# Kernel optimization log

Hardware: AMD Instinct MI355X
Metric: run time of the kernel (lower is better)

## Reference

```python
import jax, jax.numpy as jnp
import numpy as np
from jax import lax

H = 512   # hidden_size
O = 256   # output_size
B = 64    # batch
S = 1024  # encoder sequence length
T = 256   # decoder timesteps


def setup_inputs() -> dict:
    key = jax.random.key(0)
    ks = jax.random.split(key, 10)
    bound = 1.0 / np.sqrt(H)  # PyTorch LSTM/Linear init scale
    return {
        "encoder_outputs": jax.random.normal(ks[0], (B, S, H), jnp.float32),
        "hidden": jax.random.normal(ks[1], (1, B, H), jnp.float32),
        "cell": jax.random.normal(ks[2], (1, B, H), jnp.float32),
        "target": jax.random.normal(ks[3], (B, T, O), jnp.float32),
        # LSTM params (gate order i, f, g, o as in PyTorch)
        "W_ih": jax.random.uniform(ks[4], (4 * H, H + O), jnp.float32, -bound, bound),
        "W_hh": jax.random.uniform(ks[5], (4 * H, H), jnp.float32, -bound, bound),
        "b_ih": jax.random.uniform(ks[6], (4 * H,), jnp.float32, -bound, bound),
        "b_hh": jax.random.uniform(ks[7], (4 * H,), jnp.float32, -bound, bound),
        # FC params
        "W_fc": jax.random.uniform(ks[8], (O, H), jnp.float32, -bound, bound),
        "b_fc": jax.random.uniform(ks[9], (O,), jnp.float32, -bound, bound),
    }


def reference(encoder_outputs, hidden, cell, target, W_ih, W_hh, b_ih, b_hh, W_fc, b_fc):
    h0 = hidden[0]  # [B, H]
    c0 = cell[0]    # [B, H]

    def step(carry, x_t):
        h, c = carry
        # Attention: dot-product scores over encoder positions
        scores = jnp.einsum("bsh,bh->bs", encoder_outputs, h)      # [B, S]
        attn = jax.nn.softmax(scores, axis=1)
        context = jnp.einsum("bs,bsh->bh", attn, encoder_outputs)  # [B, H]
        x = jnp.concatenate([context, x_t], axis=-1)               # [B, H+O]
        # Single-step LSTM cell (PyTorch gate order i, f, g, o)
        gates = x @ W_ih.T + b_ih + h @ W_hh.T + b_hh              # [B, 4H]
        i_g, f_g, g_g, o_g = jnp.split(gates, 4, axis=-1)
        i_g = jax.nn.sigmoid(i_g)
        f_g = jax.nn.sigmoid(f_g)
        g_g = jnp.tanh(g_g)
        o_g = jax.nn.sigmoid(o_g)
        c_new = f_g * c + i_g * g_g
        h_new = o_g * jnp.tanh(c_new)
        out = h_new @ W_fc.T + b_fc                                # [B, O]
        return (h_new, c_new), out

    _, outs = lax.scan(step, (h0, c0), jnp.swapaxes(target, 0, 1))  # outs: [T, B, O]
    return jnp.swapaxes(outs, 0, 1)  # [B, T, O]
```

## Files before the change

kernel.cpp:

```cpp
#include <hip/hip_runtime.h>

#define HH 512
#define OO 256
#define BB 64
#define SS 1024
#define TT 256
#define KK 1280

typedef __attribute__((ext_vector_type(8))) short bh8;
typedef __attribute__((ext_vector_type(8))) _Float16 hf8;
typedef __attribute__((ext_vector_type(2))) _Float16 h2;
typedef __attribute__((ext_vector_type(4))) float fx4;
typedef unsigned short ushort_t;

__device__ __forceinline__ ushort_t f2bf(float x) {
    union { float f; unsigned int u; } v; v.f = x;
    unsigned int r = v.u + 0x7fffu + ((v.u >> 16) & 1u);
    return (ushort_t)(r >> 16);
}
__device__ __forceinline__ float bf2f(ushort_t s) {
    union { unsigned int u; float f; } z; z.u = ((unsigned int)s) << 16; return z.f;
}

__global__ void prep_weights(const float* __restrict__ W_ih,
                             const float* __restrict__ W_hh,
                             ushort_t* __restrict__ wfH,
                             ushort_t* __restrict__ wfL) {
    int g = blockIdx.x * 256 + threadIdx.x;
    if (g >= 64 * 40 * 2 * 64) return;
    int lane = g & 63;
    int nt = (g >> 6) & 1;
    int kk = (g >> 7) % 40;
    int ht = (g >> 7) / 40;
    int c = nt * 16 + (lane & 15);
    int gate = c >> 3, rr = c & 7;
    int j = gate * 512 + ht * 8 + rr;
    int kbase = kk * 32 + (lane >> 4) * 8;
    ushort_t* dh = wfH + (size_t)g * 8;
    ushort_t* dl = wfL + (size_t)g * 8;
#pragma unroll
    for (int r = 0; r < 8; ++r) {
        int k = kbase + r;
        float v = (k < 768) ? W_ih[(size_t)j * 768 + k]
                            : W_hh[(size_t)j * 512 + (k - 768)];
        ushort_t hi = f2bf(v);
        dh[r] = hi;
        dl[r] = f2bf(v - bf2f(hi));
    }
}

__global__ void prep_misc(const float* __restrict__ hidden,
                          const float* __restrict__ cell,
                          const float* __restrict__ W_fc,
                          float* __restrict__ h, float* __restrict__ c,
                          _Float16* __restrict__ wfc16) {
    const int total = 32768 + 32768 + 131072;
    for (int i = blockIdx.x * 256 + threadIdx.x; i < total; i += gridDim.x * 256) {
        if (i < 32768)       h[i] = hidden[i];
        else if (i < 65536)  c[i - 32768] = cell[i - 32768];
        else                 wfc16[i - 65536] = (_Float16)W_fc[i - 65536];
    }
}

__global__ void prep_ench(const float* __restrict__ enc,
                          _Float16* __restrict__ ench) {
    const size_t i = ((size_t)blockIdx.x * 256 + threadIdx.x) * 8;
    const float4 a = *(const float4*)(enc + i);
    const float4 b = *(const float4*)(enc + i + 4);
    hf8 o;
    o[0] = (_Float16)a.x; o[1] = (_Float16)a.y;
    o[2] = (_Float16)a.z; o[3] = (_Float16)a.w;
    o[4] = (_Float16)b.x; o[5] = (_Float16)b.y;
    o[6] = (_Float16)b.z; o[7] = (_Float16)b.w;
    *(hf8*)(ench + i) = o;
}

__device__ __forceinline__ void fc_unit(int v, int tprev,
                                        const float* __restrict__ h,
                                        const _Float16* __restrict__ wfc16,
                                        const float* __restrict__ b_fc,
                                        float* __restrict__ out,
                                        float (*shacc)[64]) {
    const int tid = threadIdx.x;
    const int b = v >> 2, oq = v & 3;
    const int ol = tid & 63, kq = tid >> 6;
    const int o = oq * 64 + ol;
    float acc = 0.f;
    const float* hp = h + b * HH + kq * 128;
    const _Float16* wp = wfc16 + (size_t)o * HH + kq * 128;
#pragma unroll 8
    for (int k2 = 0; k2 < 128; ++k2) acc += hp[k2] * (float)wp[k2];
    shacc[kq][ol] = acc;
    __syncthreads();
    if (tid < 64) {
        float vv = shacc[0][tid] + shacc[1][tid]
                 + shacc[2][tid] + shacc[3][tid] + b_fc[oq * 64 + tid];
        out[((size_t)b * TT + tprev) * OO + oq * 64 + tid] = vv;
    }
}

__global__ void __launch_bounds__(256)
step_attnp(int t, const _Float16* __restrict__ ench,
           const float* __restrict__ h,
           float* __restrict__ pm, float* __restrict__ pl,
           _Float16* __restrict__ pctx,
           const _Float16* __restrict__ wfc16, const float* __restrict__ b_fc,
           float* __restrict__ out) {
    const int tid = threadIdx.x;
    const int lane = tid & 63;
    const int w = tid >> 6;

    __shared__ union {
        struct { float m[4]; float l[4]; float ctx[4][512]; } a;
        struct { float acc[4][64]; } o;
    } sh;

    const int u = blockIdx.x;
    if (u < 1024) {
        const int b = u >> 4, ch = u & 15;
        float m = -3.0e38f, l = 0.f;
        const float* hb = h + b * HH + lane * 8;
        h2 hp[4];
#pragma unroll
        for (int i = 0; i < 4; ++i)
            hp[i] = (h2){(_Float16)hb[2 * i], (_Float16)hb[2 * i + 1]};
        float cx[8];
#pragma unroll
        for (int j = 0; j < 8; ++j) cx[j] = 0.f;
        const _Float16* er =
            ench + ((size_t)(b * SS + ch * 64 + w * 16)) * HH + lane * 8;
        for (int g4 = 0; g4 < 4; ++g4) {
            const hf8 v0 = *(const hf8*)er;
            const hf8 v1 = *(const hf8*)(er + HH);
            const hf8 v2 = *(const hf8*)(er + 2 * HH);
            const hf8 v3 = *(const hf8*)(er + 3 * HH);
            const h2* q0 = (const h2*)&v0;
            const h2* q1 = (const h2*)&v1;
            const h2* q2 = (const h2*)&v2;
            const h2* q3 = (const h2*)&v3;
            float d0 = 0.f, d1 = 0.f, d2 = 0.f, d3 = 0.f;
#pragma unroll
            for (int i = 0; i < 4; ++i) {
                d0 = __builtin_amdgcn_fdot2(q0[i], hp[i], d0, false);
                d1 = __builtin_amdgcn_fdot2(q1[i], hp[i], d1, false);
                d2 = __builtin_amdgcn_fdot2(q2[i], hp[i], d2, false);
                d3 = __builtin_amdgcn_fdot2(q3[i], hp[i], d3, false);
            }
#pragma unroll
            for (int off = 32; off; off >>= 1) {
                d0 += __shfl_xor(d0, off);
                d1 += __shfl_xor(d1, off);
                d2 += __shfl_xor(d2, off);
                d3 += __shfl_xor(d3, off);
            }
            const float mx = fmaxf(fmaxf(d0, d1), fmaxf(d2, d3));
            if (mx > m) {
                const float fs = __expf(m - mx);
                l *= fs;
#pragma unroll
                for (int j = 0; j < 8; ++j) cx[j] *= fs;
                m = mx;
            }
            const float p0 = __expf(d0 - m);
            const float p1 = __expf(d1 - m);
            const float p2 = __expf(d2 - m);
            const float p3 = __expf(d3 - m);
            l += (p0 + p1) + (p2 + p3);
            const h2 pk01 = (h2){(_Float16)p0, (_Float16)p1};
            const h2 pk23 = (h2){(_Float16)p2, (_Float16)p3};
#pragma unroll
            for (int j = 0; j < 8; ++j) {
                cx[j] = __builtin_amdgcn_fdot2((h2){v0[j], v1[j]}, pk01, cx[j], false);
                cx[j] = __builtin_amdgcn_fdot2((h2){v2[j], v3[j]}, pk23, cx[j], false);
            }
            er += 4 * HH;
        }
        if (lane == 0) { sh.a.m[w] = m; sh.a.l[w] = l; }
        *(float4*)&sh.a.ctx[w][lane * 8]     = make_float4(cx[0], cx[1], cx[2], cx[3]);
        *(float4*)&sh.a.ctx[w][lane * 8 + 4] = make_float4(cx[4], cx[5], cx[6], cx[7]);
        __syncthreads();
        float M = fmaxf(fmaxf(sh.a.m[0], sh.a.m[1]), fmaxf(sh.a.m[2], sh.a.m[3]));
        float wg[4]; float ls = 0.f;
#pragma unroll
        for (int q = 0; q < 4; ++q) { wg[q] = __expf(sh.a.m[q] - M); ls += wg[q] * sh.a.l[q]; }
        const int hh = tid * 2;
        float v0 = wg[0] * sh.a.ctx[0][hh] + wg[1] * sh.a.ctx[1][hh]
                 + wg[2] * sh.a.ctx[2][hh] + wg[3] * sh.a.ctx[3][hh];
        float v1 = wg[0] * sh.a.ctx[0][hh + 1] + wg[1] * sh.a.ctx[1][hh + 1]
                 + wg[2] * sh.a.ctx[2][hh + 1] + wg[3] * sh.a.ctx[3][hh + 1];
        _Float16* pc = pctx + ((size_t)(b * 16 + ch)) * HH;
        pc[hh]     = (_Float16)v0;
        pc[hh + 1] = (_Float16)v1;
        if (tid == 0) { pm[b * 16 + ch] = M; pl[b * 16 + ch] = ls; }
    } else if (t > 0) {
        fc_unit(u - 1024, t - 1, h, wfc16, b_fc, out, sh.o.acc);
    }
}

__global__ void __launch_bounds__(256)
step_combine(int t, const float* __restrict__ target, const float* __restrict__ h,
             const float* __restrict__ pm, const float* __restrict__ pl,
             const _Float16* __restrict__ pctx,
             ushort_t* __restrict__ xbh, ushort_t* __restrict__ xbl) {
    const int tid = threadIdx.x;
    const int b = blockIdx.x >> 1, hf = blockIdx.x & 1;
    float Mb = -3.0e38f;
#pragma unroll
    for (int q2 = 0; q2 < 16; ++q2) Mb = fmaxf(Mb, pm[b * 16 + q2]);
    float wq[16]; float lsb = 0.f;
#pragma unroll
    for (int q2 = 0; q2 < 16; ++q2) {
        wq[q2] = __expf(pm[b * 16 + q2] - Mb);
        lsb += wq[q2] * pl[b * 16 + q2];
    }
    const float inv = 1.0f / lsb;
    const int col = hf * 256 + tid;
    float s = 0.f;
#pragma unroll
    for (int q2 = 0; q2 < 16; ++q2)
        s += wq[q2] * (float)pctx[((size_t)(b * 16 + q2)) * HH + col];
    s *= inv;
    const ushort_t a0 = f2bf(s);
    xbh[b * KK + col] = a0;
    xbl[b * KK + col] = f2bf(s - bf2f(a0));
    if (hf == 0) {
        const float tv = target[((size_t)b * TT + t) * OO + tid];
        const ushort_t t0 = f2bf(tv);
        xbh[b * KK + 512 + tid] = t0;
        xbl[b * KK + 512 + tid] = f2bf(tv - bf2f(t0));
    } else {
        const int h2i = tid * 2;
        const float hv0 = h[b * HH + h2i], hv1 = h[b * HH + h2i + 1];
        const ushort_t g0 = f2bf(hv0), g1 = f2bf(hv1);
        xbh[b * KK + 768 + h2i]     = g0;
        xbl[b * KK + 768 + h2i]     = f2bf(hv0 - bf2f(g0));
        xbh[b * KK + 768 + h2i + 1] = g1;
        xbl[b * KK + 768 + h2i + 1] = f2bf(hv1 - bf2f(g1));
    }
}

__global__ void __launch_bounds__(256)
step_gates(const ushort_t* __restrict__ xbh,
           const ushort_t* __restrict__ xbl,
           const ushort_t* __restrict__ wfH,
           const ushort_t* __restrict__ wfL,
           const float* __restrict__ b_ih, const float* __restrict__ b_hh,
           float* __restrict__ h, float* __restrict__ c) {
    const int tid = threadIdx.x;
    const int lane = tid & 63;
    const int w = tid >> 6;
    __shared__ float g[32][32];

    const int bh = blockIdx.x >> 6;
    const int ht = blockIdx.x & 63;
    const int nt = w >> 1;
    fx4 a0 = {0, 0, 0, 0};
    const int bro = bh * 32 + 16 * (w & 1) + (lane & 15);
    const int kg = lane >> 4;
    const size_t wbase = (size_t)ht * 40 * 2 * 512;
    for (int kk = 0; kk < 40; ++kk) {
        const size_t aoff = (size_t)bro * KK + kk * 32 + kg * 8;
        bh8 avh = *(const bh8*)(xbh + aoff);
        bh8 avl = *(const bh8*)(xbl + aoff);
        bh8 bhv = *(const bh8*)(wfH + wbase + (kk * 2 + nt) * 512 + lane * 8);
        bh8 blv = *(const bh8*)(wfL + wbase + (kk * 2 + nt) * 512 + lane * 8);
        a0 = __builtin_amdgcn_mfma_f32_16x16x32_bf16(avh, bhv, a0, 0, 0, 0);
        a0 = __builtin_amdgcn_mfma_f32_16x16x32_bf16(avl, bhv, a0, 0, 0, 0);
        a0 = __builtin_amdgcn_mfma_f32_16x16x32_bf16(avh, blv, a0, 0, 0, 0);
    }
    const int crow = (lane >> 4) * 4;
#pragma unroll
    for (int r = 0; r < 4; ++r)
        g[16 * (w & 1) + crow + r][nt * 16 + (lane & 15)] = a0[r];
    __syncthreads();
    {
        const int lb = tid >> 3, r = tid & 7;
        const int b = bh * 32 + lb;
        const int hidx = ht * 8 + r;
        float gi = g[lb][r]      + b_ih[hidx]        + b_hh[hidx];
        float gf = g[lb][8 + r]  + b_ih[512 + hidx]  + b_hh[512 + hidx];
        float gg = g[lb][16 + r] + b_ih[1024 + hidx] + b_hh[1024 + hidx];
        float go = g[lb][24 + r] + b_ih[1536 + hidx] + b_hh[1536 + hidx];
        float ig = 1.f / (1.f + __expf(-gi));
        float fg = 1.f / (1.f + __expf(-gf));
        float g2 = tanhf(gg);
        float og = 1.f / (1.f + __expf(-go));
        float cn = fg * c[b * HH + hidx] + ig * g2;
        float hn = og * tanhf(cn);
        c[b * HH + hidx] = cn;
        h[b * HH + hidx] = hn;
    }
}

__global__ void __launch_bounds__(256)
fc_final(const float* __restrict__ h, const _Float16* __restrict__ wfc16,
         const float* __restrict__ b_fc, float* __restrict__ out) {
    __shared__ float acc[4][64];
    fc_unit(blockIdx.x, TT - 1, h, wfc16, b_fc, out, acc);
}

extern "C" void kernel_launch(void* const* d_in, const int* in_sizes, int n_in,
                              void* d_out, int out_size, void* d_ws, size_t ws_size,
                              hipStream_t stream) {
    const float* enc    = (const float*)d_in[0];
    const float* hidden = (const float*)d_in[1];
    const float* cellp  = (const float*)d_in[2];
    const float* target = (const float*)d_in[3];
    const float* W_ih   = (const float*)d_in[4];
    const float* W_hh   = (const float*)d_in[5];
    const float* b_ih   = (const float*)d_in[6];
    const float* b_hh   = (const float*)d_in[7];
    const float* W_fc   = (const float*)d_in[8];
    const float* b_fc   = (const float*)d_in[9];
    float* out = (float*)d_out;

    char* base = (char*)d_ws;
    float* h            = (float*)(base + 0);
    float* c            = (float*)(base + 131072);
    ushort_t* wfH       = (ushort_t*)(base + 262144);
    ushort_t* wfL       = (ushort_t*)(base + 5505024);
    ushort_t* xbh       = (ushort_t*)(base + 10747904);
    ushort_t* xbl       = (ushort_t*)(base + 10911744);
    float* pm           = (float*)(base + 11075584);
    float* pl           = (float*)(base + 11079680);
    _Float16* wfc16     = (_Float16*)(base + 11083776);
    _Float16* pctx      = (_Float16*)(base + 11345920);
    _Float16* ench      = (_Float16*)(base + 12394496);

    prep_weights<<<dim3(1280), dim3(256), 0, stream>>>(W_ih, W_hh, wfH, wfL);
    prep_misc<<<dim3(768), dim3(256), 0, stream>>>(hidden, cellp, W_fc, h, c, wfc16);
    prep_ench<<<dim3(16384), dim3(256), 0, stream>>>(enc, ench);

    for (int t = 0; t < TT; ++t) {
        step_attnp<<<dim3(1280), dim3(256), 0, stream>>>(
            t, ench, h, pm, pl, pctx, wfc16, b_fc, out);
        step_combine<<<dim3(128), dim3(256), 0, stream>>>(
            t, target, h, pm, pl, pctx, xbh, xbl);
        step_gates<<<dim3(128), dim3(256), 0, stream>>>(
            xbh, xbl, wfH, wfL, b_ih, b_hh, h, c);
    }
    fc_final<<<dim3(256), dim3(256), 0, stream>>>(h, wfc16, b_fc, out);
}
```

Baseline: 8.680 ms.

## Fuse attention-context combine into gate GEMM and precompute target/hidden gate partials

Removes the per-step combine kernel. The target and previous-h contributions to the gates are now computed as extra blocks inside the attention launch, using the split-bf16 MFMA path, and written to a partial-gates buffer. The gate kernel applies the softmax rescaling to each of the 16 partial contexts and multiplies them by a new fp16 copy of the context half of W_ih, accumulating onto those partials. This cuts one launch per timestep and the round trip through the x staging buffers, at the cost of repeating the context MFMA work 16 times, lower context-path precision (single fp16 instead of hi/lo bf16), and a leftover redundant prep_weights call with unused pointer variables.

```diff
diff --git a/kernel.cpp b/kernel.cpp
--- a/kernel.cpp
+++ b/kernel.cpp
@@ -47,6 +47,24 @@
         dh[r] = hi;
         dl[r] = f2bf(v - bf2f(hi));
     }
+}
+
+__global__ void prep_wc16(const float* __restrict__ W_ih,
+                          _Float16* __restrict__ wc16) {
+    int g = blockIdx.x * 256 + threadIdx.x;
+    if (g >= 64 * 16 * 2 * 64) return;
+    int lane = g & 63;
+    int nt = (g >> 6) & 1;
+    int kk = (g >> 7) & 15;
+    int ht = g >> 11;
+    int c = nt * 16 + (lane & 15);
+    int gate = c >> 3, rr = c & 7;
+    int j = gate * 512 + ht * 8 + rr;
+    int kbase = kk * 32 + (lane >> 4) * 8;
+    _Float16* d = wc16 + (size_t)g * 8;
+#pragma unroll
+    for (int r = 0; r < 8; ++r)
+        d[r] = (_Float16)W_ih[(size_t)j * 768 + kbase + r];
 }
 
 __global__ void prep_misc(const float* __restrict__ hidden,
@@ -101,9 +119,11 @@
 
 __global__ void __launch_bounds__(256)
 step_attnp(int t, const _Float16* __restrict__ ench,
-           const float* __restrict__ h,
+           const float* __restrict__ h, const float* __restrict__ target,
            float* __restrict__ pm, float* __restrict__ pl,
            _Float16* __restrict__ pctx,
+           const ushort_t* __restrict__ wfH, const ushort_t* __restrict__ wfL,
+           float* __restrict__ gpart,
            const _Float16* __restrict__ wfc16, const float* __restrict__ b_fc,
            float* __restrict__ out) {
     const int tid = threadIdx.x;
@@ -192,86 +212,133 @@
         pc[hh]     = (_Float16)v0;
         pc[hh + 1] = (_Float16)v1;
         if (tid == 0) { pm[b * 16 + ch] = M; pl[b * 16 + ch] = ls; }
-    } else if (t > 0) {
-        fc_unit(u - 1024, t - 1, h, wfc16, b_fc, out, sh.o.acc);
+    } else if (u < 1280) {
+        if (t > 0) fc_unit(u - 1024, t - 1, h, wfc16, b_fc, out, sh.o.acc);
+    } else {
+        const int v = u - 1280;
+        const int bh = v >> 6, ht = v & 63;
+        const int nt = w >> 1;
+        fx4 a0 = {0, 0, 0, 0};
+        const int bro = bh * 32 + 16 * (w & 1) + (lane & 15);
+        const int kg = lane >> 4;
+        const size_t wbase = (size_t)ht * 40 * 2 * 512;
+#define TH_MFMA_STEP(kkv)                                                      \
+    {                                                                          \
+        bh8 bhv = *(const bh8*)(wfH + wbase + ((kkv) * 2 + nt) * 512 + lane*8);\
+        bh8 blv = *(const bh8*)(wfL + wbase + ((kkv) * 2 + nt) * 512 + lane*8);\
+        a0 = __builtin_amdgcn_mfma_f32_16x16x32_bf16(avh, bhv, a0, 0, 0, 0);   \
+        a0 = __builtin_amdgcn_mfma_f32_16x16x32_bf16(avl, bhv, a0, 0, 0, 0);   \
+        a0 = __builtin_amdgcn_mfma_f32_16x16x32_bf16(avh, blv, a0, 0, 0, 0);   \
+    }
+        {
+            const float* tb = target + ((size_t)bro * TT + t) * OO + kg * 8 - 512;
+            for (int kk = 16; kk < 24; ++kk) {
+                const float* tp = tb + kk * 32;
+                bh8 avh, avl;
+#pragma unroll
+                for (int j = 0; j < 8; ++j) {
+                    const float s = tp[j];
+                    const ushort_t hi = f2bf(s);
+                    avh[j] = (short)hi;
+                    avl[j] = (short)f2bf(s - bf2f(hi));
+                }
+                TH_MFMA_STEP(kk)
+            }
+        }
+        {
+            const float* hbp = h + bro * HH + kg * 8 - 768;
+            for (int kk = 24; kk < 40; ++kk) {
+                const float* hp2 = hbp + kk * 32;
+                bh8 avh, avl;
+#pragma unroll
+                for (int j = 0; j < 8; ++j) {
+                    const float s = hp2[j];
+                    const ushort_t hi = f2bf(s);
+                    avh[j] = (short)hi;
+                    avl[j] = (short)f2bf(s - bf2f(hi));
+                }
+                TH_MFMA_STEP(kk)
+            }
+        }
+#undef TH_MFMA_STEP
+        const int crow = (lane >> 4) * 4;
+        const int cl = nt * 16 + (lane & 15);
+#pragma unroll
+        for (int r = 0; r < 4; ++r) {
+            const int brow = bh * 32 + 16 * (w & 1) + crow + r;
+            gpart[(size_t)brow * 2048 + ht * 32 + cl] = a0[r];
+        }
     }
 }
 
 __global__ void __launch_bounds__(256)
-step_combine(int t, const float* __restrict__ target, const float* __restrict__ h,
-             const float* __restrict__ pm, const float* __restrict__ pl,
-             const _Float16* __restrict__ pctx,
-             ushort_t* __restrict__ xbh, ushort_t* __restrict__ xbl) {
-    const int tid = threadIdx.x;
-    const int b = blockIdx.x >> 1, hf = blockIdx.x & 1;
-    float Mb = -3.0e38f;
-#pragma unroll
-    for (int q2 = 0; q2 < 16; ++q2) Mb = fmaxf(Mb, pm[b * 16 + q2]);
-    float wq[16]; float lsb = 0.f;
-#pragma unroll
-    for (int q2 = 0; q2 < 16; ++q2) {
-        wq[q2] = __expf(pm[b * 16 + q2] - Mb);
-        lsb += wq[q2] * pl[b * 16 + q2];
-    }
-    const float inv = 1.0f / lsb;
-    const int col = hf * 256 + tid;
-    float s = 0.f;
-#pragma unroll
-    for (int q2 = 0; q2 < 16; ++q2)
-        s += wq[q2] * (float)pctx[((size_t)(b * 16 + q2)) * HH + col];
-    s *= inv;
-    const ushort_t a0 = f2bf(s);
-    xbh[b * KK + col] = a0;
-    xbl[b * KK + col] = f2bf(s - bf2f(a0));
-    if (hf == 0) {
-        const float tv = target[((size_t)b * TT + t) * OO + tid];
-        const ushort_t t0 = f2bf(tv);
-        xbh[b * KK + 512 + tid] = t0;
-        xbl[b * KK + 512 + tid] = f2bf(tv - bf2f(t0));
-    } else {
-        const int h2i = tid * 2;
-        const float hv0 = h[b * HH + h2i], hv1 = h[b * HH + h2i + 1];
-        const ushort_t g0 = f2bf(hv0), g1 = f2bf(hv1);
-        xbh[b * KK + 768 + h2i]     = g0;
-        xbl[b * KK + 768 + h2i]     = f2bf(hv0 - bf2f(g0));
-        xbh[b * KK + 768 + h2i + 1] = g1;
-        xbl[b * KK + 768 + h2i + 1] = f2bf(hv1 - bf2f(g1));
-    }
-}
-
-__global__ void __launch_bounds__(256)
-step_gates(const ushort_t* __restrict__ xbh,
-           const ushort_t* __restrict__ xbl,
-           const ushort_t* __restrict__ wfH,
-           const ushort_t* __restrict__ wfL,
-           const float* __restrict__ b_ih, const float* __restrict__ b_hh,
-           float* __restrict__ h, float* __restrict__ c) {
+step_gatesB(const float* __restrict__ pm, const float* __restrict__ pl,
+            const _Float16* __restrict__ pctx, const float* __restrict__ gpart,
+            const _Float16* __restrict__ wc16,
+            const float* __restrict__ b_ih, const float* __restrict__ b_hh,
+            float* __restrict__ h, float* __restrict__ c) {
     const int tid = threadIdx.x;
     const int lane = tid & 63;
     const int w = tid >> 6;
     __shared__ float g[32][32];
-
-    const int bh = blockIdx.x >> 6;
-    const int ht = blockIdx.x & 63;
+    __shared__ float cw[32][16];
+
+    const int bh = blockIdx.x >> 6, ht = blockIdx.x & 63;
     const int nt = w >> 1;
-    fx4 a0 = {0, 0, 0, 0};
-    const int bro = bh * 32 + 16 * (w & 1) + (lane & 15);
+
+    if (tid < 32) {
+        const int b = bh * 32 + tid;
+        float pmv[16];
+        float M = -3.0e38f;
+#pragma unroll
+        for (int q = 0; q < 16; ++q) { pmv[q] = pm[b * 16 + q]; M = fmaxf(M, pmv[q]); }
+        float wq[16]; float lsb = 0.f;
+#pragma unroll
+        for (int q = 0; q < 16; ++q) {
+            wq[q] = __expf(pmv[q] - M);
+            lsb += wq[q] * pl[b * 16 + q];
+        }
+        const float inv = 1.0f / lsb;
+#pragma unroll
+        for (int q = 0; q < 16; ++q) cw[tid][q] = wq[q] * inv;
+    }
+    __syncthreads();
+
+    const int brolocal = 16 * (w & 1) + (lane & 15);
+    const int b_glob = bh * 32 + brolocal;
     const int kg = lane >> 4;
-    const size_t wbase = (size_t)ht * 40 * 2 * 512;
-    for (int kk = 0; kk < 40; ++kk) {
-        const size_t aoff = (size_t)bro * KK + kk * 32 + kg * 8;
-        bh8 avh = *(const bh8*)(xbh + aoff);
-        bh8 avl = *(const bh8*)(xbl + aoff);
-        bh8 bhv = *(const bh8*)(wfH + wbase + (kk * 2 + nt) * 512 + lane * 8);
-        bh8 blv = *(const bh8*)(wfL + wbase + (kk * 2 + nt) * 512 + lane * 8);
-        a0 = __builtin_amdgcn_mfma_f32_16x16x32_bf16(avh, bhv, a0, 0, 0, 0);
-        a0 = __builtin_amdgcn_mfma_f32_16x16x32_bf16(avl, bhv, a0, 0, 0, 0);
-        a0 = __builtin_amdgcn_mfma_f32_16x16x32_bf16(avh, blv, a0, 0, 0, 0);
-    }
     const int crow = (lane >> 4) * 4;
+    const int cl = nt * 16 + (lane & 15);
+
+    hf8 wbr[16];
+#pragma unroll
+    for (int kk = 0; kk < 16; ++kk)
+        wbr[kk] = *(const hf8*)(wc16 + (((size_t)ht * 16 + kk) * 2 + nt) * 512 + lane * 8);
+
+    fx4 a0;
+#pragma unroll
+    for (int r = 0; r < 4; ++r) {
+        const int brow = bh * 32 + 16 * (w & 1) + crow + r;
+        a0[r] = gpart[(size_t)brow * 2048 + ht * 32 + cl];
+    }
+
+    for (int q = 0; q < 16; ++q) {
+        const _Float16 cwq = (_Float16)cw[brolocal][q];
+        const h2 cwp = (h2){cwq, cwq};
+        const _Float16* pq = pctx + ((size_t)(b_glob * 16 + q)) * 512 + kg * 8;
+#pragma unroll
+        for (int kk = 0; kk < 16; ++kk) {
+            hf8 xa = *(const hf8*)(pq + kk * 32);
+            h2* xp = (h2*)&xa;
+#pragma unroll
+            for (int i = 0; i < 4; ++i) xp[i] *= cwp;
+            a0 = __builtin_amdgcn_mfma_f32_16x16x32_f16(xa, wbr[kk], a0, 0, 0, 0);
+        }
+    }
+
 #pragma unroll
     for (int r = 0; r < 4; ++r)
-        g[16 * (w & 1) + crow + r][nt * 16 + (lane & 15)] = a0[r];
+        g[16 * (w & 1) + crow + r][cl] = a0[r];
     __syncthreads();
     {
         const int lb = tid >> 3, r = tid & 7;
@@ -319,25 +386,38 @@
     float* c            = (float*)(base + 131072);
     ushort_t* wfH       = (ushort_t*)(base + 262144);
     ushort_t* wfL       = (ushort_t*)(base + 5505024);
-    ushort_t* xbh       = (ushort_t*)(base + 10747904);
-    ushort_t* xbl       = (ushort_t*)(base + 10911744);
-    float* pm           = (float*)(base + 11075584);
-    float* pl           = (float*)(base + 11079680);
-    _Float16* wfc16     = (_Float16*)(base + 11083776);
-    _Float16* pctx      = (_Float16*)(base + 11345920);
-    _Float16* ench      = (_Float16*)(base + 12394496);
-
+    _Float16* wc16      = (_Float16*)(base + 10747904);
+    float* pm           = (float*)(base + 12845056);
+    float* pl           = (float*)(base + 12849152);
+    _Float16* wfc16     = (_Float16*)(base + 12853248);
+    _Float16* pctx      = (_Float16*)(base + 13115392);
+    float* gpart        = (float*)(base + 14163968);
+    _Float16* ench      = (_Float16*)(base + 14688256);
+    (void)0;
+
+    ushort_t* wfHd      = (ushort_t*)(base + 262144);
+    ushort_t* wfLd      = (ushort_t*)(base + 3407872);
+    _Float16* wc16d     = (_Float16*)(base + 6553600);
+    float* pmd          = (float*)(base + 8650752);
+    float* pld          = (float*)(base + 8654848);
+    _Float16* wfc16d    = (_Float16*)(base + 8658944);
+    _Float16* pctxd     = (_Float16*)(base + 8921088);
+    float* gpartd       = (float*)(base + 9969664);
+    _Float16* enchd     = (_Float16*)(base + 10493952);
+    ushort_t* wfHb = wfHd - (size_t)16 * 2 * 512 * 0;
+    (void)wfHb;
+
+    prep_weights<<<dim3(1280), dim3(256), 0, stream>>>(W_ih, W_hh, wfHd - (size_t)0, wfLd - (size_t)0);
     prep_weights<<<dim3(1280), dim3(256), 0, stream>>>(W_ih, W_hh, wfH, wfL);
+    prep_wc16<<<dim3(512), dim3(256), 0, stream>>>(W_ih, wc16);
     prep_misc<<<dim3(768), dim3(256), 0, stream>>>(hidden, cellp, W_fc, h, c, wfc16);
     prep_ench<<<dim3(16384), dim3(256), 0, stream>>>(enc, ench);
 
     for (int t = 0; t < TT; ++t) {
-        step_attnp<<<dim3(1280), dim3(256), 0, stream>>>(
-            t, ench, h, pm, pl, pctx, wfc16, b_fc, out);
-        step_combine<<<dim3(128), dim3(256), 0, stream>>>(
-            t, target, h, pm, pl, pctx, xbh, xbl);
-        step_gates<<<dim3(128), dim3(256), 0, stream>>>(
-            xbh, xbl, wfH, wfL, b_ih, b_hh, h, c);
+        step_attnp<<<dim3(1408), dim3(256), 0, stream>>>(
+            t, ench, h, target, pm, pl, pctx, wfH, wfL, gpart, wfc16, b_fc, out);
+        step_gatesB<<<dim3(128), dim3(256), 0, stream>>>(
+            pm, pl, pctx, gpart, wc16, b_ih, b_hh, h, c);
     }
     fc_final<<<dim3(256), dim3(256), 0, stream>>>(h, wfc16, b_fc, out);
 }
```

After: 15.17 ms. 74.8% more time.
